# Performance work log

Hardware: AMD Instinct MI355X
Metric: run time of the kernel (lower is better)

Reference implementation:

```python
import jax, jax.numpy as jnp
import numpy as np

EPS = 1e-6
LAMBDA_INIT = 0.8

def rmsnorm(x, g):
    return x * jax.lax.rsqrt(jnp.mean(x * x, axis=-1, keepdims=True) + EPS) * g

def diff_attention(q_in, kv_in, Wq, Wk, Wv, Wo, lq1, lk1, lq2, lk2, causal):
    # q_in: [B,T,D], kv_in: [B,S,D]; Wq/Wk: [D, H*2*hs], Wv: [D, H*hs], Wo: [H*hs, D]
    B, T, _ = q_in.shape
    S = kv_in.shape[1]
    H, hs = lq1.shape
    q = (q_in @ Wq).reshape(B, T, H, 2, hs)
    k = (kv_in @ Wk).reshape(B, S, H, 2, hs)
    v = (kv_in @ Wv).reshape(B, S, H, hs)
    q1, q2 = q[..., 0, :], q[..., 1, :]
    k1, k2 = k[..., 0, :], k[..., 1, :]
    scale = 1.0 / np.sqrt(hs).astype(np.float32)
    a1 = jnp.einsum('bthd,bshd->bhts', q1, k1) * scale  # [B,H,T,S]
    a2 = jnp.einsum('bthd,bshd->bhts', q2, k2) * scale
    if causal:
        mask = jnp.tril(jnp.ones((T, S), dtype=bool))
        neg = jnp.asarray(-1e9, a1.dtype)
        a1 = jnp.where(mask, a1, neg)
        a2 = jnp.where(mask, a2, neg)
    s1 = jax.nn.softmax(a1, axis=-1)
    s2 = jax.nn.softmax(a2, axis=-1)
    lam = jnp.exp(jnp.sum(lq1 * lk1, -1)) - jnp.exp(jnp.sum(lq2 * lk2, -1)) + LAMBDA_INIT  # [H]
    attn = s1 - lam[None, :, None, None] * s2
    o = jnp.einsum('bhts,bshd->bthd', attn, v)  # [B,T,H,hs]
    # per-head RMSNorm (no affine) scaled by (1 - lambda_init), per Diff Transformer
    o = o * jax.lax.rsqrt(jnp.mean(o * o, -1, keepdims=True) + EPS) * (1.0 - LAMBDA_INIT)
    return o.reshape(B, T, H * hs) @ Wo

def swiglu(x, W1, W2, W3):
    return (jax.nn.silu(x @ W1) * (x @ W2)) @ W3

def setup_inputs():
    B, T, D, H, hs = 4, 1024, 1024, 16, 64
    Dff = 4 * D
    ks = jax.random.split(jax.random.key(0), 24)
    w = lambda i, shape, s=0.02: (jax.random.normal(ks[i], shape, jnp.float32) * s)
    return {
        'x': jax.random.normal(ks[0], (B, T, D), jnp.float32),
        'encoder_output': jax.random.normal(ks[1], (B, T, D), jnp.float32),
        'Wq_s': w(2, (D, H * 2 * hs)), 'Wk_s': w(3, (D, H * 2 * hs)),
        'Wv_s': w(4, (D, H * hs)), 'Wo_s': w(5, (H * hs, D)),
        'lq1_s': w(6, (H, hs), 0.1), 'lk1_s': w(7, (H, hs), 0.1),
        'lq2_s': w(8, (H, hs), 0.1), 'lk2_s': w(9, (H, hs), 0.1),
        'Wq_c': w(10, (D, H * 2 * hs)), 'Wk_c': w(11, (D, H * 2 * hs)),
        'Wv_c': w(12, (D, H * hs)), 'Wo_c': w(13, (H * hs, D)),
        'lq1_c': w(14, (H, hs), 0.1), 'lk1_c': w(15, (H, hs), 0.1),
        'lq2_c': w(16, (H, hs), 0.1), 'lk2_c': w(17, (H, hs), 0.1),
        'g_rms': jnp.ones((D,), jnp.float32),
        'W1': w(18, (D, Dff)), 'W2': w(19, (D, Dff)), 'W3': w(20, (Dff, D)),
    }

def reference(x, encoder_output, Wq_s, Wk_s, Wv_s, Wo_s, lq1_s, lk1_s, lq2_s, lk2_s,
              Wq_c, Wk_c, Wv_c, Wo_c, lq1_c, lk1_c, lq2_c, lk2_c,
              g_rms, W1, W2, W3):
    # dropout prob 0.0 -> identity (eval/reference mode)
    h = rmsnorm(x, g_rms)
    h = diff_attention(h, h, Wq_s, Wk_s, Wv_s, Wo_s, lq1_s, lk1_s, lq2_s, lk2_s, causal=True) + h
    h = diff_attention(h, encoder_output, Wq_c, Wk_c, Wv_c, Wo_c, lq1_c, lk1_c, lq2_c, lk2_c, causal=False)
    h = h + h  # faithful to source: out = dropout(out) + out after cross-attention
    h = swiglu(rmsnorm(h, g_rms), W1, W2, W3) + h
    return h
```

## Files before the change

kernel.cpp:

```cpp
#include <hip/hip_runtime.h>

typedef __attribute__((ext_vector_type(8))) short s16x8;
typedef __attribute__((ext_vector_type(4))) float f32x4;
typedef unsigned short u16;

__device__ __forceinline__ float bu2f(u16 u) {
    union { unsigned int i; float f; } x; x.i = ((unsigned int)u) << 16; return x.f;
}
__device__ __forceinline__ u16 f2bu(float f) {
    union { float f; unsigned int i; } x; x.f = f;
    unsigned int r = x.i + 0x7fffu + ((x.i >> 16) & 1u);
    return (u16)(r >> 16);
}

__device__ __forceinline__ void gld_lds16(const void* g, void* l) {
    __builtin_amdgcn_global_load_lds(
        (const __attribute__((address_space(1))) unsigned int*)g,
        (__attribute__((address_space(3))) unsigned int*)l, 16, 0, 0);
}
#define WAIT_LGKM0() asm volatile("s_waitcnt lgkmcnt(0)" ::: "memory")
#define MEMBAR()     asm volatile("" ::: "memory")

__global__ __launch_bounds__(256)
void transpose4_k(const float* s0, const float* s1, const float* s2, const float* s3,
                  u16* d0, u16* d1, u16* d2, u16* d3, int R, int C) {
    const float* src = blockIdx.z == 0 ? s0 : blockIdx.z == 1 ? s1 : blockIdx.z == 2 ? s2 : s3;
    u16* dst = blockIdx.z == 0 ? d0 : blockIdx.z == 1 ? d1 : blockIdx.z == 2 ? d2 : d3;
    __shared__ u16 t[32][33];
    int bx = blockIdx.x * 32, by = blockIdx.y * 32;
    int x = bx + threadIdx.x;
#pragma unroll
    for (int k = 0; k < 4; ++k)
        t[threadIdx.y + k * 8][threadIdx.x] = f2bu(src[(size_t)(by + threadIdx.y + k * 8) * C + x]);
    __syncthreads();
    int x2 = by + threadIdx.x;
#pragma unroll
    for (int k = 0; k < 4; ++k)
        dst[(size_t)(bx + threadIdx.y + k * 8) * R + x2] = t[threadIdx.x][threadIdx.y + k * 8];
}

__global__ __launch_bounds__(256)
void convert_k(const float* __restrict__ a, u16* __restrict__ o, int n4) {
    int i = blockIdx.x * 256 + threadIdx.x;
    if (i >= n4) return;
    float4 v = ((const float4*)a)[i];
    ushort4 u;
    u.x = f2bu(v.x); u.y = f2bu(v.y); u.z = f2bu(v.z); u.w = f2bu(v.w);
    ((ushort4*)o)[i] = u;
}

__global__ __launch_bounds__(256)
void rmsnorm_k(const float* __restrict__ x, const float* __restrict__ g, u16* __restrict__ y) {
    const int row = blockIdx.x, tid = threadIdx.x;
    float4 v = ((const float4*)(x + (size_t)row * 1024))[tid];
    float ss = v.x * v.x + v.y * v.y + v.z * v.z + v.w * v.w;
#pragma unroll
    for (int off = 32; off; off >>= 1) ss += __shfl_xor(ss, off, 64);
    __shared__ float red[4];
    if ((tid & 63) == 0) red[tid >> 6] = ss;
    __syncthreads();
    float tot = red[0] + red[1] + red[2] + red[3];
    float sc = rsqrtf(tot * (1.f / 1024.f) + 1e-6f);
    float4 gv = ((const float4*)g)[tid];
    ushort4 o;
    o.x = f2bu(v.x * sc * gv.x);
    o.y = f2bu(v.y * sc * gv.y);
    o.z = f2bu(v.z * sc * gv.z);
    o.w = f2bu(v.w * sc * gv.w);
    ((ushort4*)(y + (size_t)row * 1024))[tid] = o;
}

__global__ __launch_bounds__(256)
void silumul_k(const u16* __restrict__ a, const u16* __restrict__ b, u16* __restrict__ o, int n4) {
    int i = blockIdx.x * 256 + threadIdx.x;
    if (i >= n4) return;
    ushort4 ua = ((const ushort4*)a)[i], ub = ((const ushort4*)b)[i];
    ushort4 uo;
    {
        float v = bu2f(ua.x); uo.x = f2bu(v / (1.f + __expf(-v)) * bu2f(ub.x));
        v = bu2f(ua.y); uo.y = f2bu(v / (1.f + __expf(-v)) * bu2f(ub.y));
        v = bu2f(ua.z); uo.z = f2bu(v / (1.f + __expf(-v)) * bu2f(ub.z));
        v = bu2f(ua.w); uo.w = f2bu(v / (1.f + __expf(-v)) * bu2f(ub.w));
    }
    ((ushort4*)o)[i] = uo;
}

template <int TM>
__global__ __launch_bounds__(256, 2)
void gemm_bt(const u16* __restrict__ A, const u16* __restrict__ Bt, void* __restrict__ C,
             const void* __restrict__ res, int M, int N, int K, int mode) {
    constexpr int MI = TM / 32;
    __shared__ u16 sA[2][TM * 32];
    __shared__ u16 sB[2][128 * 32];
    const int tid = threadIdx.x;
    const int w = tid >> 6, lane = tid & 63, q4 = lane >> 4, l16 = lane & 15;
    const int m0 = blockIdx.y * TM, n0 = blockIdx.x * 128;
    const int wm = (w >> 1) * (TM / 2), wn = (w & 1) * 64;

    const f32x4 fzero = {0.f, 0.f, 0.f, 0.f};
    f32x4 acc[MI][4];
#pragma unroll
    for (int i = 0; i < MI; ++i)
#pragma unroll
        for (int j = 0; j < 4; ++j) acc[i][j] = fzero;

    const int r0 = tid >> 2, c0 = (tid & 3) * 8;

    auto stage = [&](int buf, int k0) {
        gld_lds16(A + (size_t)(m0 + r0) * K + k0 + c0, &sA[buf][tid * 8]);
        if (TM == 128)
            gld_lds16(A + (size_t)(m0 + 64 + r0) * K + k0 + c0, &sA[buf][(256 + tid) * 8]);
        gld_lds16(Bt + (size_t)(n0 + r0) * K + k0 + c0, &sB[buf][tid * 8]);
        gld_lds16(Bt + (size_t)(n0 + 64 + r0) * K + k0 + c0, &sB[buf][(256 + tid) * 8]);
    };

    const int nk = K >> 5;
    stage(0, 0);
    for (int it = 0; it < nk; ++it) {
        __syncthreads();
        if (it + 1 < nk) stage((it + 1) & 1, (it + 1) * 32);
        const int buf = it & 1;
        s16x8 af[MI], bfr[4];
#pragma unroll
        for (int i = 0; i < MI; ++i) af[i] = *(const s16x8*)&sA[buf][(wm + i * 16 + l16) * 32 + q4 * 8];
#pragma unroll
        for (int j = 0; j < 4; ++j) bfr[j] = *(const s16x8*)&sB[buf][(wn + j * 16 + l16) * 32 + q4 * 8];
#pragma unroll
        for (int i = 0; i < MI; ++i)
#pragma unroll
            for (int j = 0; j < 4; ++j)
                acc[i][j] = __builtin_amdgcn_mfma_f32_16x16x32_bf16(af[i], bfr[j], acc[i][j], 0, 0, 0);
        MEMBAR();
    }

    const size_t QBSZ = (size_t)4096 * 2048;
    const size_t FSZ  = (size_t)4096 * 4096;
#pragma unroll
    for (int i = 0; i < MI; ++i)
#pragma unroll
        for (int j = 0; j < 4; ++j)
#pragma unroll
            for (int r = 0; r < 4; ++r) {
                int m = m0 + wm + i * 16 + q4 * 4 + r;
                int n = n0 + wn + j * 16 + l16;
                float v = acc[i][j][r];
                if (mode == 0) {
                    ((u16*)C)[(size_t)m * N + n] = f2bu(v);
                } else if (mode == 1) {
                    ((u16*)C)[(size_t)m * N + n] = f2bu(v + bu2f(((const u16*)res)[(size_t)m * N + n]));
                } else if (mode == 2) {
                    ((float*)C)[(size_t)m * N + n] = 2.f * v;
                } else if (mode == 4) {
                    ((float*)C)[(size_t)m * N + n] = v + ((const float*)res)[(size_t)m * N + n];
                } else if (mode == 5) {
                    if (n < 2048) ((u16*)C)[(size_t)m * 2048 + n] = f2bu(v);
                    else if (n < 4096) ((u16*)C)[QBSZ + (size_t)m * 2048 + (n - 2048)] = f2bu(v);
                    else {
                        int nn = n - 4096, hh = nn >> 6, d = nn & 63, b = m >> 10, s = m & 1023;
                        ((u16*)C)[2 * QBSZ + ((size_t)((b * 16 + hh) * 64 + d)) * 1024 + s] = f2bu(v);
                    }
                } else if (mode == 6) {
                    if (n < 2048) ((u16*)C)[(size_t)m * 2048 + n] = f2bu(v);
                    else {
                        int nn = n - 2048, hh = nn >> 6, d = nn & 63, b = m >> 10, s = m & 1023;
                        ((u16*)C)[QBSZ + ((size_t)((b * 16 + hh) * 64 + d)) * 1024 + s] = f2bu(v);
                    }
                } else {
                    if (n < 4096) ((u16*)C)[(size_t)m * 4096 + n] = f2bu(v);
                    else ((u16*)C)[FSZ + (size_t)m * 4096 + (n - 4096)] = f2bu(v);
                }
            }
}

template <bool CAUSAL>
__global__ __launch_bounds__(256, 2)
void diff_flash(const u16* __restrict__ Q, const u16* __restrict__ Kg, const u16* __restrict__ Vt,
                u16* __restrict__ O, const float* __restrict__ lq1, const float* __restrict__ lk1,
                const float* __restrict__ lq2, const float* __restrict__ lk2, int T, int S) {
    __shared__ u16 sK1[2][64 * 64];
    __shared__ u16 sK2[2][64 * 64];
    __shared__ u16 sV[2][64 * 64];
    __shared__ u16 sP[4][16 * 64];

    const int tid = threadIdx.x;
    const int w = tid >> 6, lane = tid & 63, q4 = lane >> 4, l16 = lane & 15;
    const int h = blockIdx.x, b = blockIdx.y;
    const int zt = CAUSAL ? (gridDim.z - 1 - blockIdx.z) : blockIdx.z;
    const int t0 = zt * 64;
    const f32x4 fzero = {0.f, 0.f, 0.f, 0.f};

    float d1 = 0.f, d2 = 0.f;
    for (int d = 0; d < 64; ++d) {
        d1 += lq1[h * 64 + d] * lk1[h * 64 + d];
        d2 += lq2[h * 64 + d] * lk2[h * 64 + d];
    }
    const float lam = __expf(d1) - __expf(d2) + 0.8f;

    s16x8 qf[2][2];
    {
        const size_t qrow = (size_t)(b * T + t0 + w * 16 + l16) * 2048 + h * 128;
#pragma unroll
        for (int c = 0; c < 2; ++c)
#pragma unroll
            for (int kk = 0; kk < 2; ++kk)
                qf[c][kk] = *(const s16x8*)&Q[qrow + c * 64 + kk * 32 + q4 * 8];
    }

    f32x4 o1[4], o2[4];
    float ms1 = -1e30f, ls1 = 0.f, ms2 = -1e30f, ls2 = 0.f;
#pragma unroll
    for (int jn = 0; jn < 4; ++jn) { o1[jn] = fzero; o2[jn] = fzero; }

    const int ntiles = CAUSAL ? (zt + 1) : (S / 64);
    const int rk = tid >> 3;
    const int ckk = (((tid & 7) - rk) & 7) * 8;

    auto stage = [&](int buf, int s0) {
        const size_t kb = (size_t)(b * S + s0 + rk) * 2048 + h * 128;
        gld_lds16(&Kg[kb + ckk], &sK1[buf][tid * 8]);
        gld_lds16(&Kg[kb + (size_t)32 * 2048 + ckk], &sK1[buf][(256 + tid) * 8]);
        gld_lds16(&Kg[kb + 64 + ckk], &sK2[buf][tid * 8]);
        gld_lds16(&Kg[kb + (size_t)32 * 2048 + 64 + ckk], &sK2[buf][(256 + tid) * 8]);
        const size_t vb = (size_t)((b * 16 + h) * 64 + rk) * 1024 + s0;
        gld_lds16(&Vt[vb + ckk], &sV[buf][tid * 8]);
        gld_lds16(&Vt[vb + (size_t)32 * 1024 + ckk], &sV[buf][(256 + tid) * 8]);
    };

    u16* const sPw = sP[w];
    const int slot0 = ((0 * 4 + q4 + l16) & 7) * 8;
    const int slot1 = ((1 * 4 + q4 + l16) & 7) * 8;

    stage(0, 0);
    for (int it = 0; it < ntiles; ++it) {
        __syncthreads();
        if (it + 1 < ntiles) stage((it + 1) & 1, (it + 1) * 64);
        const int buf = it & 1, s0 = it * 64;
        const bool diag = CAUSAL && (it == ntiles - 1);

        s16x8 vf[4][2];
#pragma unroll
        for (int jn = 0; jn < 4; ++jn) {
            vf[jn][0] = *(const s16x8*)&sV[buf][(jn * 16 + l16) * 64 + slot0];
            vf[jn][1] = *(const s16x8*)&sV[buf][(jn * 16 + l16) * 64 + slot1];
        }

        auto comp_step = [&](const u16* sK, const s16x8* qkk, float& m, float& l, f32x4* o) {
            f32x4 sc[4];
#pragma unroll
            for (int js = 0; js < 4; ++js) sc[js] = fzero;
#pragma unroll
            for (int js = 0; js < 4; ++js) {
                s16x8 kf0 = *(const s16x8*)&sK[(js * 16 + l16) * 64 + slot0];
                sc[js] = __builtin_amdgcn_mfma_f32_16x16x32_bf16(kf0, qkk[0], sc[js], 0, 0, 0);
                s16x8 kf1 = *(const s16x8*)&sK[(js * 16 + l16) * 64 + slot1];
                sc[js] = __builtin_amdgcn_mfma_f32_16x16x32_bf16(kf1, qkk[1], sc[js], 0, 0, 0);
            }
            float p[4][4];
#pragma unroll
            for (int js = 0; js < 4; ++js)
#pragma unroll
                for (int r = 0; r < 4; ++r) {
                    float v = sc[js][r] * 0.125f;
                    if (diag && (s0 + js * 16 + q4 * 4 + r > t0 + w * 16 + l16)) v = -1e9f;
                    p[js][r] = v;
                }
            float mx = p[0][0];
#pragma unroll
            for (int js = 0; js < 4; ++js)
#pragma unroll
                for (int r = 0; r < 4; ++r) mx = fmaxf(mx, p[js][r]);
            mx = fmaxf(mx, __shfl_xor(mx, 16, 64));
            mx = fmaxf(mx, __shfl_xor(mx, 32, 64));
            float mn = fmaxf(m, mx);
            float alpha = __expf(m - mn);
            m = mn;
            float rs = 0.f;
#pragma unroll
            for (int js = 0; js < 4; ++js)
#pragma unroll
                for (int r = 0; r < 4; ++r) { p[js][r] = __expf(p[js][r] - mn); rs += p[js][r]; }
            rs += __shfl_xor(rs, 16, 64);
            rs += __shfl_xor(rs, 32, 64);
            l = l * alpha + rs;
#pragma unroll
            for (int jn = 0; jn < 4; ++jn) o[jn] *= alpha;
#pragma unroll
            for (int js = 0; js < 4; ++js) {
                ushort4 pk;
                pk.x = f2bu(p[js][0]); pk.y = f2bu(p[js][1]);
                pk.z = f2bu(p[js][2]); pk.w = f2bu(p[js][3]);
                int sl = ((js * 2 + (q4 >> 1) + l16) & 7) * 8 + (q4 & 1) * 4;
                *(ushort4*)&sPw[l16 * 64 + sl] = pk;
            }
            WAIT_LGKM0();
            s16x8 pb0 = *(const s16x8*)&sPw[l16 * 64 + slot0];
            s16x8 pb1 = *(const s16x8*)&sPw[l16 * 64 + slot1];
#pragma unroll
            for (int jn = 0; jn < 4; ++jn) {
                o[jn] = __builtin_amdgcn_mfma_f32_16x16x32_bf16(vf[jn][0], pb0, o[jn], 0, 0, 0);
                o[jn] = __builtin_amdgcn_mfma_f32_16x16x32_bf16(vf[jn][1], pb1, o[jn], 0, 0, 0);
            }
            MEMBAR();
        };
        comp_step(sK1[buf], qf[0], ms1, ls1, o1);
        comp_step(sK2[buf], qf[1], ms2, ls2, o2);
    }

    const float inv1 = 1.f / ls1, inv2 = lam / ls2;
    float val[4][4];
    float ss = 0.f;
#pragma unroll
    for (int jn = 0; jn < 4; ++jn)
#pragma unroll
        for (int r = 0; r < 4; ++r) {
            float v = o1[jn][r] * inv1 - o2[jn][r] * inv2;
            val[jn][r] = v;
            ss += v * v;
        }
    ss += __shfl_xor(ss, 16, 64);
    ss += __shfl_xor(ss, 32, 64);
    const float scl = rsqrtf(ss * (1.f / 64.f) + 1e-6f) * 0.2f;
    const size_t orow = (size_t)(b * T + t0 + w * 16 + l16) * 1024 + h * 64;
#pragma unroll
    for (int jn = 0; jn < 4; ++jn) {
        ushort4 ov;
        ov.x = f2bu(val[jn][0] * scl); ov.y = f2bu(val[jn][1] * scl);
        ov.z = f2bu(val[jn][2] * scl); ov.w = f2bu(val[jn][3] * scl);
        *(ushort4*)&O[orow + jn * 16 + q4 * 4] = ov;
    }
}

extern "C" void kernel_launch(void* const* d_in, const int* in_sizes, int n_in,
                              void* d_out, int out_size, void* d_ws, size_t ws_size,
                              hipStream_t stream) {
    (void)in_sizes; (void)n_in; (void)out_size; (void)ws_size;
    const float* x     = (const float*)d_in[0];
    const float* enc   = (const float*)d_in[1];
    const float* Wq_s  = (const float*)d_in[2];
    const float* Wk_s  = (const float*)d_in[3];
    const float* Wv_s  = (const float*)d_in[4];
    const float* Wo_s  = (const float*)d_in[5];
    const float* lq1_s = (const float*)d_in[6];
    const float* lk1_s = (const float*)d_in[7];
    const float* lq2_s = (const float*)d_in[8];
    const float* lk2_s = (const float*)d_in[9];
    const float* Wq_c  = (const float*)d_in[10];
    const float* Wk_c  = (const float*)d_in[11];
    const float* Wv_c  = (const float*)d_in[12];
    const float* Wo_c  = (const float*)d_in[13];
    const float* lq1_c = (const float*)d_in[14];
    const float* lk1_c = (const float*)d_in[15];
    const float* lq2_c = (const float*)d_in[16];
    const float* lk2_c = (const float*)d_in[17];
    const float* g_rms = (const float*)d_in[18];
    const float* W1    = (const float*)d_in[19];
    const float* W2    = (const float*)d_in[20];
    const float* W3    = (const float*)d_in[21];

    char* ws = (char*)d_ws;
    size_t off = 0;
    auto ab = [&](size_t elems) -> u16* { u16* p = (u16*)(ws + off); off += elems * 2; return p; };
    u16* WqkvTs = ab((size_t)5120 * 1024);
    u16* WoTs   = ab((size_t)1024 * 1024);
    u16* WqTc   = ab((size_t)2048 * 1024);
    u16* WkvTc  = ab((size_t)3072 * 1024);
    u16* WoTc   = ab((size_t)1024 * 1024);
    u16* W12T   = ab((size_t)8192 * 1024);
    u16* W3T    = ab((size_t)1024 * 4096);
    char* pool = ws + off;
    u16* h0   = ab((size_t)4096 * 1024);
    u16* encb = ab((size_t)4096 * 1024);
    u16* Qb   = ab((size_t)4096 * 2048);
    u16* Kb   = ab((size_t)4096 * 2048);
    u16* Vt   = ab((size_t)4096 * 1024);
    u16* Ob   = ab((size_t)4096 * 1024);
    u16* fa   = (u16*)pool;
    u16* fb   = (u16*)(pool + (size_t)4096 * 4096 * 2);
    u16* h1   = ab((size_t)4096 * 1024);
    float* h2 = (float*)(ws + off); off += (size_t)4096 * 1024 * 4;
    u16* rn   = ab((size_t)4096 * 1024);

    dim3 tb(32, 8);
    transpose4_k<<<dim3(64, 32, 4), tb, 0, stream>>>(
        Wq_s, Wk_s, Wq_c, Wk_c,
        WqkvTs, WqkvTs + (size_t)2048 * 1024, WqTc, WkvTc, 1024, 2048);
    transpose4_k<<<dim3(32, 32, 4), tb, 0, stream>>>(
        Wv_s, Wo_s, Wv_c, Wo_c,
        WqkvTs + (size_t)4096 * 1024, WoTs, WkvTc + (size_t)2048 * 1024, WoTc, 1024, 1024);
    transpose4_k<<<dim3(128, 32, 2), tb, 0, stream>>>(
        W1, W2, W1, W2, W12T, W12T + (size_t)4096 * 1024, W12T, W12T, 1024, 4096);
    transpose4_k<<<dim3(32, 128, 1), tb, 0, stream>>>(W3, W3, W3, W3, W3T, W3T, W3T, W3T, 4096, 1024);

    rmsnorm_k<<<4096, 256, 0, stream>>>(x, g_rms, h0);
    convert_k<<<4096, 256, 0, stream>>>(enc, encb, 4096 * 1024 / 4);

    gemm_bt<128><<<dim3(40, 32), 256, 0, stream>>>(h0, WqkvTs, Qb, nullptr, 4096, 5120, 1024, 5);
    diff_flash<true><<<dim3(16, 4, 16), 256, 0, stream>>>(Qb, Kb, Vt, Ob, lq1_s, lk1_s, lq2_s, lk2_s, 1024, 1024);
    gemm_bt<64><<<dim3(8, 64), 256, 0, stream>>>(Ob, WoTs, h1, h0, 4096, 1024, 1024, 1);

    gemm_bt<128><<<dim3(16, 32), 256, 0, stream>>>(h1, WqTc, Qb, nullptr, 4096, 2048, 1024, 0);
    gemm_bt<128><<<dim3(24, 32), 256, 0, stream>>>(encb, WkvTc, Kb, nullptr, 4096, 3072, 1024, 6);
    diff_flash<false><<<dim3(16, 4, 16), 256, 0, stream>>>(Qb, Kb, Vt, Ob, lq1_c, lk1_c, lq2_c, lk2_c, 1024, 1024);
    gemm_bt<64><<<dim3(8, 64), 256, 0, stream>>>(Ob, WoTc, h2, nullptr, 4096, 1024, 1024, 2);

    rmsnorm_k<<<4096, 256, 0, stream>>>(h2, g_rms, rn);
    gemm_bt<128><<<dim3(64, 32), 256, 0, stream>>>(rn, W12T, fa, nullptr, 4096, 8192, 1024, 7);
    silumul_k<<<16384, 256, 0, stream>>>(fa, fb, fa, 4096 * 4096 / 4);
    gemm_bt<64><<<dim3(8, 64), 256, 0, stream>>>(fa, W3T, (float*)d_out, h2, 4096, 1024, 4096, 4);
}
```

Measured before the change: 785.7 us.

## Add 256x256-tile GEMM kernel with swizzled LDS and XCD-aware block mapping

Introduces a new 512-thread GEMM using 256x256 output tiles, XOR-swizzled LDS layout for bank-conflict-free fragment loads, a block-index remap that groups tiles per XCD, interleaved global-to-LDS prefetch with explicit vmcnt waits and barriers, and s_setprio around MFMA bursts. The large-N projection GEMMs (QKV, cross Q, cross KV, W1/W2) switch to it, while the N=1024 GEMMs keep the old kernel. The epilogue store logic is factored into a shared helper. Larger tiles raise arithmetic intensity per LDS byte but use many accumulator registers and leave fewer blocks to fill the GPU for the smaller GEMMs.

```diff
diff --git a/kernel.cpp b/kernel.cpp
--- a/kernel.cpp
+++ b/kernel.cpp
@@ -20,6 +20,9 @@
 }
 #define WAIT_LGKM0() asm volatile("s_waitcnt lgkmcnt(0)" ::: "memory")
 #define MEMBAR()     asm volatile("" ::: "memory")
+#define VMCNT4()     asm volatile("s_waitcnt vmcnt(4)" ::: "memory")
+#define VMCNT0()     asm volatile("s_waitcnt vmcnt(0)" ::: "memory")
+#define SBAR()       asm volatile("s_barrier" ::: "memory")
 
 __global__ __launch_bounds__(256)
 void transpose4_k(const float* s0, const float* s1, const float* s2, const float* s3,
@@ -85,6 +88,141 @@
     ((ushort4*)o)[i] = uo;
 }
 
+__device__ __forceinline__ void gemm_store(void* __restrict__ C, const void* __restrict__ res,
+                                           int N, int mode, int m, int n, float v) {
+    const size_t QBSZ = (size_t)4096 * 2048;
+    const size_t FSZ  = (size_t)4096 * 4096;
+    if (mode == 0) {
+        ((u16*)C)[(size_t)m * N + n] = f2bu(v);
+    } else if (mode == 1) {
+        ((u16*)C)[(size_t)m * N + n] = f2bu(v + bu2f(((const u16*)res)[(size_t)m * N + n]));
+    } else if (mode == 2) {
+        ((float*)C)[(size_t)m * N + n] = 2.f * v;
+    } else if (mode == 4) {
+        ((float*)C)[(size_t)m * N + n] = v + ((const float*)res)[(size_t)m * N + n];
+    } else if (mode == 5) {
+        if (n < 2048) ((u16*)C)[(size_t)m * 2048 + n] = f2bu(v);
+        else if (n < 4096) ((u16*)C)[QBSZ + (size_t)m * 2048 + (n - 2048)] = f2bu(v);
+        else {
+            int nn = n - 4096, hh = nn >> 6, d = nn & 63, b = m >> 10, s = m & 1023;
+            ((u16*)C)[2 * QBSZ + ((size_t)((b * 16 + hh) * 64 + d)) * 1024 + s] = f2bu(v);
+        }
+    } else if (mode == 6) {
+        if (n < 2048) ((u16*)C)[(size_t)m * 2048 + n] = f2bu(v);
+        else {
+            int nn = n - 2048, hh = nn >> 6, d = nn & 63, b = m >> 10, s = m & 1023;
+            ((u16*)C)[QBSZ + ((size_t)((b * 16 + hh) * 64 + d)) * 1024 + s] = f2bu(v);
+        }
+    } else {
+        if (n < 4096) ((u16*)C)[(size_t)m * 4096 + n] = f2bu(v);
+        else ((u16*)C)[FSZ + (size_t)m * 4096 + (n - 4096)] = f2bu(v);
+    }
+}
+
+__global__ __launch_bounds__(512, 2)
+void gemm256(const u16* __restrict__ A, const u16* __restrict__ Bt, void* __restrict__ C,
+             const void* __restrict__ res, int M, int N, int K, int mode) {
+    __shared__ u16 sA[2][256 * 32];
+    __shared__ u16 sB[2][256 * 32];
+
+    const int tid = threadIdx.x;
+    const int w = tid >> 6, lane = tid & 63, q4 = lane >> 4, l16 = lane & 15;
+    const int wr = w >> 2, wc = w & 3;
+    const int wm = wr * 128, wn = wc * 64;
+
+    const int nx = N >> 8;
+    const int nwg = gridDim.x;
+    const int cpx = nwg >> 3;
+    const int bid = blockIdx.x;
+    const int sw = (bid & 7) * cpx + (bid >> 3);
+    const int bx = sw % nx, by = sw / nx;
+    const int m0 = by << 8, n0 = bx << 8;
+
+    const int koff = (((tid & 3) ^ ((tid >> 3) & 3)) << 3);
+    const size_t aR0 = (size_t)(m0 + (tid >> 2)) * K;
+    const size_t aR1 = aR0 + (size_t)128 * K;
+    const size_t bR0 = (size_t)(n0 + (tid >> 2)) * K;
+    const size_t bR1 = bR0 + (size_t)128 * K;
+    const int dst0 = tid * 8, dst1 = (512 + tid) * 8;
+
+    auto stageA = [&](int kh, int ke) {
+        gld_lds16(A + aR0 + ke + koff, &sA[kh][dst0]);
+        gld_lds16(A + aR1 + ke + koff, &sA[kh][dst1]);
+    };
+    auto stageB = [&](int kh, int ke) {
+        gld_lds16(Bt + bR0 + ke + koff, &sB[kh][dst0]);
+        gld_lds16(Bt + bR1 + ke + koff, &sB[kh][dst1]);
+    };
+
+    const f32x4 fzero = {0.f, 0.f, 0.f, 0.f};
+    f32x4 acc[8][4];
+#pragma unroll
+    for (int i = 0; i < 8; ++i)
+#pragma unroll
+        for (int j = 0; j < 4; ++j) acc[i][j] = fzero;
+
+    s16x8 af[8], bf[4];
+    const int fsl = ((q4 ^ ((l16 >> 1) & 3)) << 3);
+
+    auto loadfrags = [&](int kh) {
+        const u16* pa = &sA[kh][0];
+        const u16* pb = &sB[kh][0];
+#pragma unroll
+        for (int mm = 0; mm < 8; ++mm)
+            af[mm] = *(const s16x8*)&pa[(wm + mm * 16 + l16) * 32 + fsl];
+#pragma unroll
+        for (int nn = 0; nn < 4; ++nn)
+            bf[nn] = *(const s16x8*)&pb[(wn + nn * 16 + l16) * 32 + fsl];
+    };
+    auto mfma16 = [&](int nb) {
+        __builtin_amdgcn_s_setprio(1);
+#pragma unroll
+        for (int mm = 0; mm < 8; ++mm) {
+            acc[mm][nb]     = __builtin_amdgcn_mfma_f32_16x16x32_bf16(af[mm], bf[nb],     acc[mm][nb],     0, 0, 0);
+            acc[mm][nb + 1] = __builtin_amdgcn_mfma_f32_16x16x32_bf16(af[mm], bf[nb + 1], acc[mm][nb + 1], 0, 0, 0);
+        }
+        __builtin_amdgcn_s_setprio(0);
+        MEMBAR();
+    };
+
+    const int nt = K >> 6;
+    stageA(0, 0); stageB(0, 0); stageA(1, 32); stageB(1, 32);
+
+    for (int t = 0; t < nt; ++t) {
+        const int kb = (t + 1) << 6;
+        const bool pf = (t + 1 < nt);
+        VMCNT4();
+        SBAR();
+        loadfrags(0);
+        WAIT_LGKM0();
+        mfma16(0);
+        SBAR();
+        if (pf) stageA(0, kb);
+        mfma16(2);
+        SBAR();
+        if (pf) { stageB(0, kb); VMCNT4(); } else { VMCNT0(); }
+        SBAR();
+        loadfrags(1);
+        WAIT_LGKM0();
+        mfma16(0);
+        SBAR();
+        if (pf) { stageA(1, kb + 32); stageB(1, kb + 32); }
+        mfma16(2);
+        SBAR();
+    }
+
+#pragma unroll
+    for (int mm = 0; mm < 8; ++mm)
+#pragma unroll
+        for (int nn = 0; nn < 4; ++nn)
+#pragma unroll
+            for (int r = 0; r < 4; ++r) {
+                int m = m0 + wm + mm * 16 + q4 * 4 + r;
+                int n = n0 + wn + nn * 16 + l16;
+                gemm_store(C, res, N, mode, m, n, acc[mm][nn][r]);
+            }
+}
+
 template <int TM>
 __global__ __launch_bounds__(256, 2)
 void gemm_bt(const u16* __restrict__ A, const u16* __restrict__ Bt, void* __restrict__ C,
@@ -133,8 +271,6 @@
         MEMBAR();
     }
 
-    const size_t QBSZ = (size_t)4096 * 2048;
-    const size_t FSZ  = (size_t)4096 * 4096;
 #pragma unroll
     for (int i = 0; i < MI; ++i)
 #pragma unroll
@@ -143,32 +279,7 @@
             for (int r = 0; r < 4; ++r) {
                 int m = m0 + wm + i * 16 + q4 * 4 + r;
                 int n = n0 + wn + j * 16 + l16;
-                float v = acc[i][j][r];
-                if (mode == 0) {
-                    ((u16*)C)[(size_t)m * N + n] = f2bu(v);
-                } else if (mode == 1) {
-                    ((u16*)C)[(size_t)m * N + n] = f2bu(v + bu2f(((const u16*)res)[(size_t)m * N + n]));
-                } else if (mode == 2) {
-                    ((float*)C)[(size_t)m * N + n] = 2.f * v;
-                } else if (mode == 4) {
-                    ((float*)C)[(size_t)m * N + n] = v + ((const float*)res)[(size_t)m * N + n];
-                } else if (mode == 5) {
-                    if (n < 2048) ((u16*)C)[(size_t)m * 2048 + n] = f2bu(v);
-                    else if (n < 4096) ((u16*)C)[QBSZ + (size_t)m * 2048 + (n - 2048)] = f2bu(v);
-                    else {
-                        int nn = n - 4096, hh = nn >> 6, d = nn & 63, b = m >> 10, s = m & 1023;
-                        ((u16*)C)[2 * QBSZ + ((size_t)((b * 16 + hh) * 64 + d)) * 1024 + s] = f2bu(v);
-                    }
-                } else if (mode == 6) {
-                    if (n < 2048) ((u16*)C)[(size_t)m * 2048 + n] = f2bu(v);
-                    else {
-                        int nn = n - 2048, hh = nn >> 6, d = nn & 63, b = m >> 10, s = m & 1023;
-                        ((u16*)C)[QBSZ + ((size_t)((b * 16 + hh) * 64 + d)) * 1024 + s] = f2bu(v);
-                    }
-                } else {
-                    if (n < 4096) ((u16*)C)[(size_t)m * 4096 + n] = f2bu(v);
-                    else ((u16*)C)[FSZ + (size_t)m * 4096 + (n - 4096)] = f2bu(v);
-                }
+                gemm_store(C, res, N, mode, m, n, acc[i][j][r]);
             }
 }
 
@@ -394,17 +505,17 @@
     rmsnorm_k<<<4096, 256, 0, stream>>>(x, g_rms, h0);
     convert_k<<<4096, 256, 0, stream>>>(enc, encb, 4096 * 1024 / 4);
 
-    gemm_bt<128><<<dim3(40, 32), 256, 0, stream>>>(h0, WqkvTs, Qb, nullptr, 4096, 5120, 1024, 5);
+    gemm256<<<dim3(20 * 16), 512, 0, stream>>>(h0, WqkvTs, Qb, nullptr, 4096, 5120, 1024, 5);
     diff_flash<true><<<dim3(16, 4, 16), 256, 0, stream>>>(Qb, Kb, Vt, Ob, lq1_s, lk1_s, lq2_s, lk2_s, 1024, 1024);
     gemm_bt<64><<<dim3(8, 64), 256, 0, stream>>>(Ob, WoTs, h1, h0, 4096, 1024, 1024, 1);
 
-    gemm_bt<128><<<dim3(16, 32), 256, 0, stream>>>(h1, WqTc, Qb, nullptr, 4096, 2048, 1024, 0);
-    gemm_bt<128><<<dim3(24, 32), 256, 0, stream>>>(encb, WkvTc, Kb, nullptr, 4096, 3072, 1024, 6);
+    gemm256<<<dim3(8 * 16), 512, 0, stream>>>(h1, WqTc, Qb, nullptr, 4096, 2048, 1024, 0);
+    gemm256<<<dim3(12 * 16), 512, 0, stream>>>(encb, WkvTc, Kb, nullptr, 4096, 3072, 1024, 6);
     diff_flash<false><<<dim3(16, 4, 16), 256, 0, stream>>>(Qb, Kb, Vt, Ob, lq1_c, lk1_c, lq2_c, lk2_c, 1024, 1024);
     gemm_bt<64><<<dim3(8, 64), 256, 0, stream>>>(Ob, WoTc, h2, nullptr, 4096, 1024, 1024, 2);
 
     rmsnorm_k<<<4096, 256, 0, stream>>>(h2, g_rms, rn);
-    gemm_bt<128><<<dim3(64, 32), 256, 0, stream>>>(rn, W12T, fa, nullptr, 4096, 8192, 1024, 7);
+    gemm256<<<dim3(32 * 16), 512, 0, stream>>>(rn, W12T, fa, nullptr, 4096, 8192, 1024, 7);
     silumul_k<<<16384, 256, 0, stream>>>(fa, fb, fa, 4096 * 4096 / 4);
     gemm_bt<64><<<dim3(8, 64), 256, 0, stream>>>(fa, W3T, (float*)d_out, h2, 4096, 1024, 4096, 4);
 }
```

Measured after the change: 974.7 us. +24.0%, slower.
